# Optimization experiments

Hardware: AMD Instinct MI355X
Metric: run time of the kernel (lower is better)

Reference implementation:

```python
import jax, jax.numpy as jnp
import numpy as np

B = 512        # batch
D = 128        # embedding_dim (n_input)
S = 50         # max_tweets_num (n_sequence)
T = 32         # max_seq_len (n_steps)
HOOPS = 2
NUM_USERS = 20000
NUM_ITEMS = 100000
LATENT = 64
NUM_FRIENDS = 10000
CLIP = 50      # friend_clip
PAD = 50000    # vocab.pad; word table has PAD+1 rows


def setup_inputs() -> dict:
    key = jax.random.key(0)
    ks = jax.random.split(key, 24)
    s = 0.02
    emb_word = (jax.random.normal(ks[0], (PAD + 1, D)) * s).at[PAD].set(0.0)
    emb_item = jax.random.normal(ks[1], (NUM_ITEMS, LATENT)) * s
    emb_user = (jax.random.normal(ks[2], (NUM_FRIENDS + 1, LATENT)) * s).at[NUM_FRIENDS].set(0.0)
    W_mem = jax.random.normal(ks[3], (LATENT, D)) * s
    b_mem = jnp.zeros((D,))
    w_word = jax.random.normal(ks[4], (D,)) * s
    b_word = jnp.zeros(())
    w_sent = jax.random.normal(ks[5], (D,)) * s
    b_sent = jnp.zeros(())
    W_tr = jax.random.normal(ks[6], (D, LATENT)) * s
    b_tr = jnp.zeros((LATENT,))
    W1 = jax.random.normal(ks[7], (LATENT, LATENT // 2)) * s
    b1 = jnp.zeros((LATENT // 2,))
    W2 = jax.random.normal(ks[8], (LATENT // 2, LATENT // 4)) * s
    b2 = jnp.zeros((LATENT // 4,))
    W3 = jax.random.normal(ks[9], (LATENT // 4, 2)) * s
    b3 = jnp.zeros((2,))
    w_aff = jax.random.normal(ks[10], (LATENT,)) * s
    b_aff = jnp.zeros(())
    user_tweet_indices = jax.random.randint(ks[11], (NUM_USERS, S, T), 0, PAD)
    ufi = jax.random.randint(ks[12], (NUM_USERS, CLIP), 0, NUM_FRIENDS)
    # simulate padded friend lists in the trailing slots
    user_friend_indices = ufi.at[:, CLIP - 5:].set(NUM_FRIENDS)
    user_indices = jax.random.randint(ks[13], (B,), 0, NUM_USERS)
    item_indices = jax.random.randint(ks[14], (B,), 0, NUM_ITEMS)
    return {
        'user_indices': user_indices, 'item_indices': item_indices,
        'emb_word': emb_word, 'emb_item': emb_item, 'emb_user': emb_user,
        'W_mem': W_mem, 'b_mem': b_mem, 'w_word': w_word, 'b_word': b_word,
        'w_sent': w_sent, 'b_sent': b_sent, 'W_tr': W_tr, 'b_tr': b_tr,
        'W1': W1, 'b1': b1, 'W2': W2, 'b2': b2, 'W3': W3, 'b3': b3,
        'w_aff': w_aff, 'b_aff': b_aff,
        'user_tweet_indices': user_tweet_indices,
        'user_friend_indices': user_friend_indices,
    }


def reference(user_indices, item_indices, emb_word, emb_item, emb_user,
              W_mem, b_mem, w_word, b_word, w_sent, b_sent, W_tr, b_tr,
              W1, b1, W2, b2, W3, b3, w_aff, b_aff,
              user_tweet_indices, user_friend_indices):
    item_emb = emb_item[item_indices]                       # [B, L]
    mem = item_emb @ W_mem + b_mem                          # [B, D]
    tweets = emb_word[user_tweet_indices[user_indices]]     # [B, S, T, D]
    for _ in range(HOOPS):
        # word-level attention: scores via broadcast mul+sum == einsum
        ww = jax.nn.softmax(jnp.einsum('bstd,bd->bst', tweets, mem), axis=2)
        sentence = jnp.einsum('bst,bstd->bsd', ww, tweets)  # [B, S, D]
        sw = sentence @ w_word + b_word                     # [B, S]
        iw = mem @ w_sent + b_sent                          # [B]
        swf = jax.nn.softmax(jnp.tanh(sw + iw[:, None]), axis=1)
        mem = jnp.einsum('bs,bsd->bd', swf, sentence) + mem
    ept = mem @ W_tr + b_tr                                 # [B, L]
    fidx = user_friend_indices[user_indices]                # [B, C]
    femb = emb_user[fidx]                                   # [B, C, L]
    friend_num = CLIP - (fidx == NUM_FRIENDS).sum(axis=1, keepdims=True).astype(jnp.float32)
    group_idx = jax.nn.sigmoid(
        jnp.einsum('bcl,l->bc', item_emb[:, None, :] * femb, w_aff) + b_aff)[..., None]
    femb = femb * group_idx
    user_emb = femb.sum(axis=1) / friend_num                # [B, L]
    a = jax.nn.sigmoid(item_emb @ W1 + b1)
    a = jax.nn.sigmoid(a @ W2 + b2)
    alpha = jax.nn.sigmoid(a @ W3 + b3)                     # [B, 2]
    vector = alpha[:, 0:1] * ept + alpha[:, 1:2] * user_emb
    rating = jax.nn.sigmoid((vector * item_emb) @ w_aff + b_aff)  # [B]
    return rating, group_idx
```

## Files before the change

kernel.cpp:

```cpp
#include <hip/hip_runtime.h>
#include <hip/hip_fp16.h>

#define NB 512
#define DD 128
#define SS 50
#define TT 32
#define LL 64
#define CLIPN 50
#define NFRIENDS 10000
#define NTHREADS 512
#define NWAVES 8
#define PAD1 50001
#define WELEMS (PAD1 * DD)

typedef unsigned short u16;
typedef unsigned int u32;
typedef _Float16 h2 __attribute__((ext_vector_type(2)));
typedef __fp16 hf2 __attribute__((ext_vector_type(2)));

__device__ __forceinline__ float bf2f(u32 u) {
    union { u32 i; float f; } c; c.i = u << 16; return c.f;
}
__device__ __forceinline__ u16 f2bf(float f) {
    union { float f; u32 i; } c; c.f = f;
    u32 x = c.i;
    return (u16)((x + 0x7fffu + ((x >> 16) & 1u)) >> 16);
}
__device__ __forceinline__ float sigf(float x) { return 1.f / (1.f + expf(-x)); }

__device__ __forceinline__ h2 u2h(u32 x) { union { u32 u; h2 h; } c; c.u = x; return c.h; }
__device__ __forceinline__ u32 h2u(h2 x) { union { h2 h; u32 u; } c; c.h = x; return c.u; }
__device__ __forceinline__ h2 pkrtz(float a, float b) {
    union { hf2 p; h2 h; } c; c.p = __builtin_amdgcn_cvt_pkrtz(a, b); return c.h;
}
__device__ __forceinline__ h2 declo(u32 w) {
    return u2h(__builtin_amdgcn_perm(w, 0u, 0x05010400u));
}
__device__ __forceinline__ h2 dechi(u32 w) {
    return u2h(__builtin_amdgcn_perm(w, 0u, 0x07010600u));
}
#define FD2(a, b, c) __builtin_amdgcn_fdot2((a), (b), (c), false)

__device__ __forceinline__ u32 e5m2_byte(float x) {
    u16 h = __half_as_ushort(__float2half(x));
    u16 r = (u16)(h + 0x7Fu + ((h >> 8) & 1u));
    return (r >> 8) & 0xffu;
}
__device__ __forceinline__ u32 e5m2_enc4(const float* v) {
    return e5m2_byte(v[0]) | (e5m2_byte(v[1]) << 8) |
           (e5m2_byte(v[2]) << 16) | (e5m2_byte(v[3]) << 24);
}

template <bool BF16> struct LD;
template <> struct LD<true> {
    static __device__ __forceinline__ float one(const void* p, long i) {
        return bf2f(((const u16*)p)[i]);
    }
    static __device__ __forceinline__ void st(void* p, long i, float v) {
        ((u16*)p)[i] = f2bf(v);
    }
};
template <> struct LD<false> {
    static __device__ __forceinline__ float one(const void* p, long i) {
        return ((const float*)p)[i];
    }
    static __device__ __forceinline__ void st(void* p, long i, float v) {
        ((float*)p)[i] = v;
    }
};

template <int WM> struct WT;
template <> struct WT<0> {
    static __device__ __forceinline__ void sixteen(const void* p, long i, float* o) {
        const float* s = (const float*)p + i;
        #pragma unroll
        for (int j = 0; j < 4; ++j) {
            float4 v = *(const float4*)(s + 4 * j);
            o[4*j] = v.x; o[4*j+1] = v.y; o[4*j+2] = v.z; o[4*j+3] = v.w;
        }
    }
    static __device__ __forceinline__ void four(const void* p, long i, float* o) {
        float4 v = *(const float4*)((const float*)p + i);
        o[0] = v.x; o[1] = v.y; o[2] = v.z; o[3] = v.w;
    }
};
template <> struct WT<1> {
    static __device__ __forceinline__ void sixteen(const void* p, long i, float* o) {
        const u16* s = (const u16*)p + i;
        #pragma unroll
        for (int j = 0; j < 2; ++j) {
            uint4 v = *(const uint4*)(s + 8 * j);
            float* q = o + 8 * j;
            q[0] = bf2f(v.x & 0xffffu); q[1] = bf2f(v.x >> 16);
            q[2] = bf2f(v.y & 0xffffu); q[3] = bf2f(v.y >> 16);
            q[4] = bf2f(v.z & 0xffffu); q[5] = bf2f(v.z >> 16);
            q[6] = bf2f(v.w & 0xffffu); q[7] = bf2f(v.w >> 16);
        }
    }
    static __device__ __forceinline__ void four(const void* p, long i, float* o) {
        uint2 v = *(const uint2*)((const u16*)p + i);
        o[0] = bf2f(v.x & 0xffffu); o[1] = bf2f(v.x >> 16);
        o[2] = bf2f(v.y & 0xffffu); o[3] = bf2f(v.y >> 16);
    }
};

__device__ __forceinline__ int sniff_wave(const u16* p, int lane) {
    int bad = 0;
    #pragma unroll
    for (int j = 0; j < 8; ++j) {
        unsigned e = (p[lane * 8 + j] >> 7) & 0xffu;
        bad += (e >= 127u);
    }
    #pragma unroll
    for (int off = 1; off < 64; off <<= 1) bad += __shfl_xor(bad, off, 64);
    return (bad <= 16) ? 1 : 0;
}

__global__ void convert_words(const void* __restrict__ src, u32* __restrict__ dst) {
    __shared__ int s_flag;
    if (threadIdx.x < 64) {
        int f = sniff_wave((const u16*)src, (int)threadIdx.x);
        if (threadIdx.x == 0) s_flag = f;
    }
    __syncthreads();
    long idx = (long)blockIdx.x * 256 + threadIdx.x;
    long i = idx * 16;
    if (i >= WELEMS) return;
    float v[16];
    if (s_flag == 0) {
        const float* s = (const float*)src + i;
        #pragma unroll
        for (int j = 0; j < 4; ++j) {
            float4 q = *(const float4*)(s + 4 * j);
            v[4*j] = q.x; v[4*j+1] = q.y; v[4*j+2] = q.z; v[4*j+3] = q.w;
        }
    } else {
        WT<1>::sixteen(src, i, v);
    }
    uint4 o;
    o.x = e5m2_enc4(v); o.y = e5m2_enc4(v + 4);
    o.z = e5m2_enc4(v + 8); o.w = e5m2_enc4(v + 12);
    *(uint4*)(dst + idx * 4) = o;
}

template <bool BF16>
__global__ __launch_bounds__(NTHREADS, 4)
void nrs_fast(const int* __restrict__ user_idx,
              const int* __restrict__ item_idx,
              const void* __restrict__ wtab,
              const void* __restrict__ emb_item,
              const void* __restrict__ emb_user,
              const void* __restrict__ W_mem, const void* __restrict__ b_mem,
              const void* __restrict__ w_word, const void* __restrict__ b_word,
              const void* __restrict__ w_sent, const void* __restrict__ b_sent,
              const void* __restrict__ W_tr, const void* __restrict__ b_tr,
              const void* __restrict__ W1, const void* __restrict__ b1,
              const void* __restrict__ W2, const void* __restrict__ b2,
              const void* __restrict__ W3, const void* __restrict__ b3,
              const void* __restrict__ w_aff, const void* __restrict__ b_aff,
              const int* __restrict__ uti, const int* __restrict__ ufi,
              void* __restrict__ out,
              const void* __restrict__ ew_raw)
{
    __shared__ float s_mem[DD];
    __shared__ float s_item[LL];
    __shared__ float s_sent[SS * DD];
    __shared__ int   s_uti[SS * TT];
    __shared__ float s_sw[SS];
    __shared__ float s_swf[SS];
    __shared__ float s_q[LL];
    __shared__ float s_ept[LL];
    __shared__ float s_uemb[LL];
    __shared__ int   s_fidx[CLIPN];
    __shared__ float s_g[CLIPN];
    __shared__ float s_a1[32];
    __shared__ float s_a2[16];
    __shared__ float s_alpha[2];
    __shared__ float s_fnum;
    __shared__ int   s_flag;
    __shared__ uint4 s_tile[NWAVES * TT * 8];

    const int b = blockIdx.x;
    const int tid = (int)threadIdx.x;
    const int lane = tid & 63;
    const int wave = tid >> 6;

    if (tid < 64) {
        int f = sniff_wave((const u16*)ew_raw, lane);
        if (tid == 0) s_flag = f;
    }
    __syncthreads();
    if (s_flag != (BF16 ? 1 : 0)) return;

    const int u = user_idx[b];
    const int it = item_idx[b];
    const long utb = (long)u * (SS * TT);

    if (tid < LL) s_item[tid] = LD<BF16>::one(emb_item, (long)it * LL + tid);
    __syncthreads();

    for (int i = tid; i < SS * TT; i += NTHREADS) s_uti[i] = uti[utb + i];
    if (tid < DD) {
        float acc = LD<BF16>::one(b_mem, tid);
        #pragma unroll 8
        for (int l = 0; l < LL; ++l)
            acc += s_item[l] * LD<BF16>::one(W_mem, l * DD + tid);
        s_mem[tid] = acc;
    }
    __syncthreads();

    const float bw = LD<BF16>::one(b_word, 0);
    const float bs = LD<BF16>::one(b_sent, 0);
    const int t = lane >> 1, h = lane & 1;
    const int dq = lane & 31, th = lane >> 5;
    const int ctop = dq >> 2, cw = dq & 3;
    float ww4[4];
    #pragma unroll
    for (int k = 0; k < 4; ++k) ww4[k] = LD<BF16>::one(w_word, 4 * dq + k);
    const float ws0 = LD<BF16>::one(w_sent, lane);
    const float ws1 = LD<BF16>::one(w_sent, lane + 64);

    uint4* const twave = s_tile + wave * (TT * 8);
    const u32* const trp = (const u32*)twave;
    h2 memh[32];

    for (int hoop = 0; hoop < 2; ++hoop) {
        {
            const float* mrow = &s_mem[h * 64];
            #pragma unroll
            for (int k = 0; k < 32; ++k)
                memh[k] = pkrtz(mrow[2 * k], mrow[2 * k + 1]);
        }

        for (int s = wave; s < SS; s += NWAVES) {
            const int row = s_uti[s * TT + t];
            const uint4* gp = (const uint4*)((const char*)wtab + ((row << 7) + (h << 6)));
            uint4 w[4];
            #pragma unroll
            for (int j = 0; j < 4; ++j) w[j] = gp[j];

            {
                const int swz = t & 7;
                uint4* tp = twave + t * 8;
                #pragma unroll
                for (int j = 0; j < 4; ++j) tp[(h * 4 + j) ^ swz] = w[j];
            }

            float acc = 0.f;
            #pragma unroll
            for (int j = 0; j < 4; ++j) {
                acc = FD2(declo(w[j].x), memh[8*j + 0], acc);
                acc = FD2(dechi(w[j].x), memh[8*j + 1], acc);
                acc = FD2(declo(w[j].y), memh[8*j + 2], acc);
                acc = FD2(dechi(w[j].y), memh[8*j + 3], acc);
                acc = FD2(declo(w[j].z), memh[8*j + 4], acc);
                acc = FD2(dechi(w[j].z), memh[8*j + 5], acc);
                acc = FD2(declo(w[j].w), memh[8*j + 6], acc);
                acc = FD2(dechi(w[j].w), memh[8*j + 7], acc);
            }
            acc += __shfl_xor(acc, 1, 64);

            float mx = acc;
            #pragma unroll
            for (int off = 2; off < 64; off <<= 1) mx = fmaxf(mx, __shfl_xor(mx, off, 64));
            float e = expf(acc - mx);
            float sm = e;
            #pragma unroll
            for (int off = 2; off < 64; off <<= 1) sm += __shfl_xor(sm, off, 64);
            const float wwt = e / sm;

            __threadfence_block();
            h2 pa0 = u2h(0u), pa1 = u2h(0u);
            #pragma unroll
            for (int i2 = 0; i2 < 16; ++i2) {
                const int t2 = th * 16 + i2;
                float wv = __shfl(wwt, 2 * t2, 64);
                h2 wh = pkrtz(wv, wv);
                u32 wrd = trp[t2 * 32 + ((ctop ^ (t2 & 7)) << 2) + cw];
                pa0 += declo(wrd) * wh;
                pa1 += dechi(wrd) * wh;
            }
            pa0 += u2h((u32)__shfl_xor((int)h2u(pa0), 32, 64));
            pa1 += u2h((u32)__shfl_xor((int)h2u(pa1), 32, 64));
            const float f0 = (float)pa0.x, f1 = (float)pa0.y;
            const float f2 = (float)pa1.x, f3 = (float)pa1.y;
            if (th == 0)
                *(float4*)&s_sent[s * DD + 4 * dq] = make_float4(f0, f1, f2, f3);

            float p = f0 * ww4[0] + f1 * ww4[1] + f2 * ww4[2] + f3 * ww4[3];
            #pragma unroll
            for (int off = 1; off < 32; off <<= 1) p += __shfl_xor(p, off, 64);
            if (lane == 0) s_sw[s] = p + bw;
        }
        __syncthreads();

        if (wave == 0) {
            float p = s_mem[lane] * ws0 + s_mem[lane + 64] * ws1;
            #pragma unroll
            for (int off = 1; off < 64; off <<= 1) p += __shfl_xor(p, off, 64);
            float iw = p + bs;
            float v = (lane < SS) ? tanhf(s_sw[lane] + iw) : -2.f;
            float mx = v;
            #pragma unroll
            for (int off = 1; off < 64; off <<= 1) mx = fmaxf(mx, __shfl_xor(mx, off, 64));
            float e = (lane < SS) ? expf(v - mx) : 0.f;
            float sm = e;
            #pragma unroll
            for (int off = 1; off < 64; off <<= 1) sm += __shfl_xor(sm, off, 64);
            if (lane < SS) s_swf[lane] = e / sm;
        }
        __syncthreads();

        if (tid < DD) {
            float acc = s_mem[tid];
            for (int s2 = 0; s2 < SS; ++s2)
                acc += s_swf[s2] * s_sent[s2 * DD + tid];
            s_mem[tid] = acc;
        }
        __syncthreads();
    }

    if (tid < LL) {
        float acc = LD<BF16>::one(b_tr, tid);
        for (int d = 0; d < DD; ++d)
            acc += s_mem[d] * LD<BF16>::one(W_tr, d * LL + tid);
        s_ept[tid] = acc;
    } else if (tid < 128) {
        int l = tid - 64;
        s_q[l] = s_item[l] * LD<BF16>::one(w_aff, l);
    } else if (tid < 128 + CLIPN) {
        s_fidx[tid - 128] = ufi[(long)u * CLIPN + (tid - 128)];
    } else if (tid >= 192 && tid < 224) {
        int j = tid - 192;
        float acc = LD<BF16>::one(b1, j);
        for (int l = 0; l < LL; ++l)
            acc += s_item[l] * LD<BF16>::one(W1, l * 32 + j);
        s_a1[j] = sigf(acc);
    }
    __syncthreads();

    const float baff = LD<BF16>::one(b_aff, 0);
    if (tid < CLIPN) {
        long fb = (long)s_fidx[tid] * LL;
        float acc = 0.f;
        for (int l = 0; l < LL; ++l) acc += LD<BF16>::one(emb_user, fb + l) * s_q[l];
        float g = sigf(acc + baff);
        s_g[tid] = g;
        LD<BF16>::st(out, NB + (long)b * CLIPN + tid, g);
    } else if (tid >= 64 && tid < 80) {
        int j = tid - 64;
        float acc = LD<BF16>::one(b2, j);
        for (int k = 0; k < 32; ++k) acc += s_a1[k] * LD<BF16>::one(W2, k * 16 + j);
        s_a2[j] = sigf(acc);
    } else if (tid == 80) {
        int cnt = 0;
        for (int c = 0; c < CLIPN; ++c) cnt += (s_fidx[c] == NFRIENDS);
        s_fnum = (float)(CLIPN - cnt);
    }
    __syncthreads();

    if (tid >= 64 && tid < 128) {
        int l = tid - 64;
        float acc = 0.f;
        for (int c = 0; c < CLIPN; ++c)
            acc += s_g[c] * LD<BF16>::one(emb_user, (long)s_fidx[c] * LL + l);
        s_uemb[l] = acc;
    } else if (tid < 2) {
        float acc = LD<BF16>::one(b3, tid);
        for (int k = 0; k < 16; ++k) acc += s_a2[k] * LD<BF16>::one(W3, k * 2 + tid);
        s_alpha[tid] = sigf(acc);
    }
    __syncthreads();

    if (wave == 0) {
        float vec = s_alpha[0] * s_ept[lane] + s_alpha[1] * (s_uemb[lane] / s_fnum);
        float p = vec * s_q[lane];
        #pragma unroll
        for (int off = 1; off < 64; off <<= 1) p += __shfl_xor(p, off, 64);
        if (lane == 0) LD<BF16>::st(out, b, sigf(p + baff));
    }
}

template <bool BF16, int WM>
__global__ __launch_bounds__(NTHREADS, 4)
void nrs_generic(const int* __restrict__ user_idx,
                 const int* __restrict__ item_idx,
                 const void* __restrict__ wtab,
                 const void* __restrict__ emb_item,
                 const void* __restrict__ emb_user,
                 const void* __restrict__ W_mem, const void* __restrict__ b_mem,
                 const void* __restrict__ w_word, const void* __restrict__ b_word,
                 const void* __restrict__ w_sent, const void* __restrict__ b_sent,
                 const void* __restrict__ W_tr, const void* __restrict__ b_tr,
                 const void* __restrict__ W1, const void* __restrict__ b1,
                 const void* __restrict__ W2, const void* __restrict__ b2,
                 const void* __restrict__ W3, const void* __restrict__ b3,
                 const void* __restrict__ w_aff, const void* __restrict__ b_aff,
                 const int* __restrict__ uti, const int* __restrict__ ufi,
                 void* __restrict__ out)
{
    __shared__ float s_mem[DD];
    __shared__ float s_item[LL];
    __shared__ float s_sent[SS * DD];
    __shared__ int   s_uti[SS * TT];
    __shared__ float s_sw[SS];
    __shared__ float s_swf[SS];
    __shared__ float s_q[LL];
    __shared__ float s_ept[LL];
    __shared__ float s_uemb[LL];
    __shared__ int   s_fidx[CLIPN];
    __shared__ float s_g[CLIPN];
    __shared__ float s_a1[32];
    __shared__ float s_a2[16];
    __shared__ float s_alpha[2];
    __shared__ float s_fnum;
    __shared__ int   s_flag;

    const int b = blockIdx.x;
    const int tid = (int)threadIdx.x;
    const int lane = tid & 63;
    const int wave = tid >> 6;

    if (tid < 64) {
        int f = sniff_wave((const u16*)wtab, lane);
        if (tid == 0) s_flag = f;
    }
    __syncthreads();
    if (s_flag != (BF16 ? 1 : 0)) return;

    const int u = user_idx[b];
    const int it = item_idx[b];
    const long utb = (long)u * (SS * TT);

    if (tid < LL) s_item[tid] = LD<BF16>::one(emb_item, (long)it * LL + tid);
    __syncthreads();

    for (int i = tid; i < SS * TT; i += NTHREADS) s_uti[i] = uti[utb + i];
    if (tid < DD) {
        float acc = LD<BF16>::one(b_mem, tid);
        #pragma unroll 8
        for (int l = 0; l < LL; ++l)
            acc += s_item[l] * LD<BF16>::one(W_mem, l * DD + tid);
        s_mem[tid] = acc;
    }
    __syncthreads();

    const float bw = LD<BF16>::one(b_word, 0);
    const float bs = LD<BF16>::one(b_sent, 0);
    const int dq = lane & 31;
    const int th = lane >> 5;
    float ww4[4];
    #pragma unroll
    for (int k = 0; k < 4; ++k) ww4[k] = LD<BF16>::one(w_word, 4 * dq + k);
    const float ws0 = LD<BF16>::one(w_sent, lane);
    const float ws1 = LD<BF16>::one(w_sent, lane + 64);

    for (int hoop = 0; hoop < 2; ++hoop) {
        for (int s = wave; s < SS; s += NWAVES) {
            const int t = lane >> 1, h = lane & 1;
            const int row = s_uti[s * TT + t];
            const long base = (long)row * DD + h * 64;
            float acc = 0.f;
            #pragma unroll
            for (int j = 0; j < 4; ++j) {
                float v16[16];
                WT<WM>::sixteen(wtab, base + 16 * j, v16);
                const float* mp = &s_mem[h * 64 + 16 * j];
                #pragma unroll
                for (int k = 0; k < 16; ++k) acc += v16[k] * mp[k];
            }
            acc += __shfl_xor(acc, 1, 64);

            float mx = acc;
            #pragma unroll
            for (int off = 1; off < 64; off <<= 1) mx = fmaxf(mx, __shfl_xor(mx, off, 64));
            float e = expf(acc - mx);
            float sm = e;
            #pragma unroll
            for (int off = 1; off < 64; off <<= 1) sm += __shfl_xor(sm, off, 64);
            float wwt = 2.f * e / sm;

            float a4[4] = {0.f, 0.f, 0.f, 0.f};
            #pragma unroll 4
            for (int i2 = 0; i2 < 16; ++i2) {
                int t2 = th * 16 + i2;
                float wv = __shfl(wwt, 2 * t2, 64);
                int r2 = s_uti[s * TT + t2];
                float v4[4];
                WT<WM>::four(wtab, (long)r2 * DD + 4 * dq, v4);
                #pragma unroll
                for (int k = 0; k < 4; ++k) a4[k] += wv * v4[k];
            }
            #pragma unroll
            for (int k = 0; k < 4; ++k) a4[k] += __shfl_xor(a4[k], 32, 64);
            if (th == 0)
                *(float4*)&s_sent[s * DD + 4 * dq] =
                    make_float4(a4[0], a4[1], a4[2], a4[3]);

            float p = a4[0] * ww4[0] + a4[1] * ww4[1] + a4[2] * ww4[2] + a4[3] * ww4[3];
            #pragma unroll
            for (int off = 1; off < 64; off <<= 1) p += __shfl_xor(p, off, 64);
            if (lane == 0) s_sw[s] = 0.5f * p + bw;
        }
        __syncthreads();

        if (wave == 0) {
            float p = s_mem[lane] * ws0 + s_mem[lane + 64] * ws1;
            #pragma unroll
            for (int off = 1; off < 64; off <<= 1) p += __shfl_xor(p, off, 64);
            float iw = p + bs;
            float v = (lane < SS) ? tanhf(s_sw[lane] + iw) : -2.f;
            float mx = v;
            #pragma unroll
            for (int off = 1; off < 64; off <<= 1) mx = fmaxf(mx, __shfl_xor(mx, off, 64));
            float e = (lane < SS) ? expf(v - mx) : 0.f;
            float sm = e;
            #pragma unroll
            for (int off = 1; off < 64; off <<= 1) sm += __shfl_xor(sm, off, 64);
            if (lane < SS) s_swf[lane] = e / sm;
        }
        __syncthreads();

        if (tid < DD) {
            float acc = s_mem[tid];
            for (int s2 = 0; s2 < SS; ++s2)
                acc += s_swf[s2] * s_sent[s2 * DD + tid];
            s_mem[tid] = acc;
        }
        __syncthreads();
    }

    if (tid < LL) {
        float acc = LD<BF16>::one(b_tr, tid);
        for (int d = 0; d < DD; ++d)
            acc += s_mem[d] * LD<BF16>::one(W_tr, d * LL + tid);
        s_ept[tid] = acc;
    } else if (tid < 128) {
        int l = tid - 64;
        s_q[l] = s_item[l] * LD<BF16>::one(w_aff, l);
    } else if (tid < 128 + CLIPN) {
        s_fidx[tid - 128] = ufi[(long)u * CLIPN + (tid - 128)];
    } else if (tid >= 192 && tid < 224) {
        int j = tid - 192;
        float acc = LD<BF16>::one(b1, j);
        for (int l = 0; l < LL; ++l)
            acc += s_item[l] * LD<BF16>::one(W1, l * 32 + j);
        s_a1[j] = sigf(acc);
    }
    __syncthreads();

    const float baff = LD<BF16>::one(b_aff, 0);
    if (tid < CLIPN) {
        long fb = (long)s_fidx[tid] * LL;
        float acc = 0.f;
        for (int l = 0; l < LL; ++l) acc += LD<BF16>::one(emb_user, fb + l) * s_q[l];
        float g = sigf(acc + baff);
        s_g[tid] = g;
        LD<BF16>::st(out, NB + (long)b * CLIPN + tid, g);
    } else if (tid >= 64 && tid < 80) {
        int j = tid - 64;
        float acc = LD<BF16>::one(b2, j);
        for (int k = 0; k < 32; ++k) acc += s_a1[k] * LD<BF16>::one(W2, k * 16 + j);
        s_a2[j] = sigf(acc);
    } else if (tid == 80) {
        int cnt = 0;
        for (int c = 0; c < CLIPN; ++c) cnt += (s_fidx[c] == NFRIENDS);
        s_fnum = (float)(CLIPN - cnt);
    }
    __syncthreads();

    if (tid >= 64 && tid < 128) {
        int l = tid - 64;
        float acc = 0.f;
        for (int c = 0; c < CLIPN; ++c)
            acc += s_g[c] * LD<BF16>::one(emb_user, (long)s_fidx[c] * LL + l);
        s_uemb[l] = acc;
    } else if (tid < 2) {
        float acc = LD<BF16>::one(b3, tid);
        for (int k = 0; k < 16; ++k) acc += s_a2[k] * LD<BF16>::one(W3, k * 2 + tid);
        s_alpha[tid] = sigf(acc);
    }
    __syncthreads();

    if (wave == 0) {
        float vec = s_alpha[0] * s_ept[lane] + s_alpha[1] * (s_uemb[lane] / s_fnum);
        float p = vec * s_q[lane];
        #pragma unroll
        for (int off = 1; off < 64; off <<= 1) p += __shfl_xor(p, off, 64);
        if (lane == 0) LD<BF16>::st(out, b, sigf(p + baff));
    }
}

extern "C" void kernel_launch(void* const* d_in, const int* in_sizes, int n_in,
                              void* d_out, int out_size, void* d_ws, size_t ws_size,
                              hipStream_t stream) {
    (void)in_sizes; (void)n_in; (void)out_size;
    u32* wbuf = (u32*)d_ws;
    const bool ws_ok = ws_size >= (size_t)WELEMS;

    if (ws_ok) {
        const long nthr = (WELEMS + 15) / 16;
        convert_words<<<(int)((nthr + 255) / 256), 256, 0, stream>>>(d_in[2], wbuf);
        nrs_fast<true><<<NB, NTHREADS, 0, stream>>>(
            (const int*)d_in[0], (const int*)d_in[1], (const void*)wbuf,
            d_in[3], d_in[4], d_in[5], d_in[6], d_in[7], d_in[8], d_in[9],
            d_in[10], d_in[11], d_in[12], d_in[13], d_in[14], d_in[15],
            d_in[16], d_in[17], d_in[18], d_in[19], d_in[20],
            (const int*)d_in[21], (const int*)d_in[22], d_out, d_in[2]);
        nrs_fast<false><<<NB, NTHREADS, 0, stream>>>(
            (const int*)d_in[0], (const int*)d_in[1], (const void*)wbuf,
            d_in[3], d_in[4], d_in[5], d_in[6], d_in[7], d_in[8], d_in[9],
            d_in[10], d_in[11], d_in[12], d_in[13], d_in[14], d_in[15],
            d_in[16], d_in[17], d_in[18], d_in[19], d_in[20],
            (const int*)d_in[21], (const int*)d_in[22], d_out, d_in[2]);
    } else {
        nrs_generic<true, 1><<<NB, NTHREADS, 0, stream>>>(
            (const int*)d_in[0], (const int*)d_in[1], d_in[2],
            d_in[3], d_in[4], d_in[5], d_in[6], d_in[7], d_in[8], d_in[9],
            d_in[10], d_in[11], d_in[12], d_in[13], d_in[14], d_in[15],
            d_in[16], d_in[17], d_in[18], d_in[19], d_in[20],
            (const int*)d_in[21], (const int*)d_in[22], d_out);
        nrs_generic<false, 0><<<NB, NTHREADS, 0, stream>>>(
            (const int*)d_in[0], (const int*)d_in[1], d_in[2],
            d_in[3], d_in[4], d_in[5], d_in[6], d_in[7], d_in[8], d_in[9],
            d_in[10], d_in[11], d_in[12], d_in[13], d_in[14], d_in[15],
            d_in[16], d_in[17], d_in[18], d_in[19], d_in[20],
            (const int*)d_in[21], (const int*)d_in[22], d_out);
    }
}
```

Baseline: 276.6 us.

## Prefetch next sentence rows, drop softmax max-reductions, stage word weights in LDS

Software-pipelines the word-embedding gather so that the next sentence's rows are loaded while the current one is processed. It also removes the max-subtraction reductions in both softmaxes, relying on the logits being small, and switches to the fast __expf. The per-token attention weights go to a small LDS array read back as float4, replacing 16 cross-lane shuffles. Dot-product and accumulation chains are split into independent partial sums to expose ILP. The cost is extra registers for the prefetch buffer and a risk of overflow if logits ever become large.

```diff
diff --git a/kernel.cpp b/kernel.cpp
--- a/kernel.cpp
+++ b/kernel.cpp
@@ -26,7 +26,7 @@
     u32 x = c.i;
     return (u16)((x + 0x7fffu + ((x >> 16) & 1u)) >> 16);
 }
-__device__ __forceinline__ float sigf(float x) { return 1.f / (1.f + expf(-x)); }
+__device__ __forceinline__ float sigf(float x) { return 1.f / (1.f + __expf(-x)); }
 
 __device__ __forceinline__ h2 u2h(u32 x) { union { u32 u; h2 h; } c; c.u = x; return c.h; }
 __device__ __forceinline__ u32 h2u(h2 x) { union { h2 h; u32 u; } c; c.h = x; return c.u; }
@@ -178,6 +178,7 @@
     __shared__ float s_alpha[2];
     __shared__ float s_fnum;
     __shared__ int   s_flag;
+    __shared__ float s_ww[NWAVES][TT];
     __shared__ uint4 s_tile[NWAVES * TT * 8];
 
     const int b = blockIdx.x;
@@ -232,12 +233,25 @@
                 memh[k] = pkrtz(mrow[2 * k], mrow[2 * k + 1]);
         }
 
+        uint4 w[4];
+        {
+            const int row0 = s_uti[wave * TT + t];
+            const uint4* gp0 = (const uint4*)((const char*)wtab +
+                                              ((row0 << 7) + (h << 6)));
+            #pragma unroll
+            for (int j = 0; j < 4; ++j) w[j] = gp0[j];
+        }
+
         for (int s = wave; s < SS; s += NWAVES) {
-            const int row = s_uti[s * TT + t];
-            const uint4* gp = (const uint4*)((const char*)wtab + ((row << 7) + (h << 6)));
-            uint4 w[4];
-            #pragma unroll
-            for (int j = 0; j < 4; ++j) w[j] = gp[j];
+            uint4 wn[4];
+            {
+                const int sn = (s + NWAVES < SS) ? (s + NWAVES) : s;
+                const int rown = s_uti[sn * TT + t];
+                const uint4* gpn = (const uint4*)((const char*)wtab +
+                                                  ((rown << 7) + (h << 6)));
+                #pragma unroll
+                for (int j = 0; j < 4; ++j) wn[j] = gpn[j];
+            }
 
             {
                 const int swz = t & 7;
@@ -246,40 +260,55 @@
                 for (int j = 0; j < 4; ++j) tp[(h * 4 + j) ^ swz] = w[j];
             }
 
-            float acc = 0.f;
+            float a0 = 0.f, a1 = 0.f, a2 = 0.f, a3 = 0.f;
             #pragma unroll
             for (int j = 0; j < 4; ++j) {
-                acc = FD2(declo(w[j].x), memh[8*j + 0], acc);
-                acc = FD2(dechi(w[j].x), memh[8*j + 1], acc);
-                acc = FD2(declo(w[j].y), memh[8*j + 2], acc);
-                acc = FD2(dechi(w[j].y), memh[8*j + 3], acc);
-                acc = FD2(declo(w[j].z), memh[8*j + 4], acc);
-                acc = FD2(dechi(w[j].z), memh[8*j + 5], acc);
-                acc = FD2(declo(w[j].w), memh[8*j + 6], acc);
-                acc = FD2(dechi(w[j].w), memh[8*j + 7], acc);
+                float* ap = (j == 0) ? &a0 : (j == 1) ? &a1 : (j == 2) ? &a2 : &a3;
+                float ac = *ap;
+                ac = FD2(declo(w[j].x), memh[8*j + 0], ac);
+                ac = FD2(dechi(w[j].x), memh[8*j + 1], ac);
+                ac = FD2(declo(w[j].y), memh[8*j + 2], ac);
+                ac = FD2(dechi(w[j].y), memh[8*j + 3], ac);
+                ac = FD2(declo(w[j].z), memh[8*j + 4], ac);
+                ac = FD2(dechi(w[j].z), memh[8*j + 5], ac);
+                ac = FD2(declo(w[j].w), memh[8*j + 6], ac);
+                ac = FD2(dechi(w[j].w), memh[8*j + 7], ac);
+                *ap = ac;
             }
+            float acc = (a0 + a1) + (a2 + a3);
             acc += __shfl_xor(acc, 1, 64);
 
-            float mx = acc;
-            #pragma unroll
-            for (int off = 2; off < 64; off <<= 1) mx = fmaxf(mx, __shfl_xor(mx, off, 64));
-            float e = expf(acc - mx);
+            float e = __expf(acc);
             float sm = e;
             #pragma unroll
             for (int off = 2; off < 64; off <<= 1) sm += __shfl_xor(sm, off, 64);
             const float wwt = e / sm;
+            if (h == 0) s_ww[wave][t] = wwt;
+
+            h2 wh2[16];
+            {
+                const float* wp = &s_ww[wave][th * 16];
+                #pragma unroll
+                for (int jj = 0; jj < 4; ++jj) {
+                    float4 q = *(const float4*)(wp + 4 * jj);
+                    wh2[4*jj+0] = pkrtz(q.x, q.x);
+                    wh2[4*jj+1] = pkrtz(q.y, q.y);
+                    wh2[4*jj+2] = pkrtz(q.z, q.z);
+                    wh2[4*jj+3] = pkrtz(q.w, q.w);
+                }
+            }
 
             __threadfence_block();
-            h2 pa0 = u2h(0u), pa1 = u2h(0u);
+            h2 p0a = u2h(0u), p0b = u2h(0u), p1a = u2h(0u), p1b = u2h(0u);
             #pragma unroll
             for (int i2 = 0; i2 < 16; ++i2) {
                 const int t2 = th * 16 + i2;
-                float wv = __shfl(wwt, 2 * t2, 64);
-                h2 wh = pkrtz(wv, wv);
-                u32 wrd = trp[t2 * 32 + ((ctop ^ (t2 & 7)) << 2) + cw];
-                pa0 += declo(wrd) * wh;
-                pa1 += dechi(wrd) * wh;
+                const u32 wrd = trp[t2 * 32 + ((ctop ^ (i2 & 7)) << 2) + cw];
+                const h2 wh = wh2[i2];
+                if (i2 & 1) { p0b += declo(wrd) * wh; p1b += dechi(wrd) * wh; }
+                else        { p0a += declo(wrd) * wh; p1a += dechi(wrd) * wh; }
             }
+            h2 pa0 = p0a + p0b, pa1 = p1a + p1b;
             pa0 += u2h((u32)__shfl_xor((int)h2u(pa0), 32, 64));
             pa1 += u2h((u32)__shfl_xor((int)h2u(pa1), 32, 64));
             const float f0 = (float)pa0.x, f1 = (float)pa0.y;
@@ -291,6 +320,9 @@
             #pragma unroll
             for (int off = 1; off < 32; off <<= 1) p += __shfl_xor(p, off, 64);
             if (lane == 0) s_sw[s] = p + bw;
+
+            #pragma unroll
+            for (int j = 0; j < 4; ++j) w[j] = wn[j];
         }
         __syncthreads();
 
@@ -299,11 +331,7 @@
             #pragma unroll
             for (int off = 1; off < 64; off <<= 1) p += __shfl_xor(p, off, 64);
             float iw = p + bs;
-            float v = (lane < SS) ? tanhf(s_sw[lane] + iw) : -2.f;
-            float mx = v;
-            #pragma unroll
-            for (int off = 1; off < 64; off <<= 1) mx = fmaxf(mx, __shfl_xor(mx, off, 64));
-            float e = (lane < SS) ? expf(v - mx) : 0.f;
+            float e = (lane < SS) ? __expf(tanhf(s_sw[lane] + iw)) : 0.f;
             float sm = e;
             #pragma unroll
             for (int off = 1; off < 64; off <<= 1) sm += __shfl_xor(sm, off, 64);
```

Result: no change. 275.2 us (-0.5%).
